# Kernel optimization log

Measured on AMD Instinct MI355X. Metric: run time of the kernel, lower is better.

## Reference

```python
import jax, jax.numpy as jnp
import numpy as np

H = 1024   # hidden_size
NH = 16    # num heads
DH = H // NH
L = 2      # attention levels
E = 8      # experts
F = 4 * H  # expert FFN hidden
B = 2
S = 1024
EPS = 1e-5
TOPK = 2
STD = 0.02


def setup_inputs() -> dict:
    key = jax.random.key(0)
    ks = jax.random.split(key, 12)
    def n(k, shp):
        return jax.random.normal(k, shp, jnp.float32) * STD
    return {
        "hidden_states": jax.random.normal(ks[0], (B, S, H), jnp.float32),
        "attention_mask": jnp.ones((B, S), jnp.int32),
        "ln1_g": jnp.ones((H,), jnp.float32), "ln1_b": jnp.zeros((H,), jnp.float32),
        "ln2_g": jnp.ones((H,), jnp.float32), "ln2_b": jnp.zeros((H,), jnp.float32),
        "Wq": n(ks[1], (L, H, H)), "Wk": n(ks[2], (L, H, H)),
        "Wv": n(ks[3], (L, H, H)), "Wo": n(ks[4], (L, H, H)),
        "bq": jnp.zeros((L, H), jnp.float32), "bk": jnp.zeros((L, H), jnp.float32),
        "bv": jnp.zeros((L, H), jnp.float32), "bo": jnp.zeros((L, H), jnp.float32),
        "level_logits": n(ks[5], (L,)),
        "Wr": n(ks[6], (H, E)), "br": jnp.zeros((E,), jnp.float32),
        "W1": n(ks[7], (E, H, F)), "b1": jnp.zeros((E, F), jnp.float32),
        "W2": n(ks[8], (E, F, H)), "b2": jnp.zeros((E, H), jnp.float32),
    }


def _ln(x, g, b):
    m = x.mean(-1, keepdims=True)
    v = x.var(-1, keepdims=True)
    return (x - m) * jax.lax.rsqrt(v + EPS) * g + b


def _mla(x, mask_f, Wq, Wk, Wv, Wo, bq, bk, bv, bo, level_logits):
    # Multi-level attention: one MHA per level, softmax-combined over levels.
    b_, s_, _ = x.shape
    def proj(W, bias):
        y = jnp.einsum('bsh,lhd->lbsd', x, W) + bias[:, None, None, :]
        return y.reshape(L, b_, s_, NH, DH)
    q, k, v = proj(Wq, bq), proj(Wk, bk), proj(Wv, bv)
    scores = jnp.einsum('lbqnd,lbknd->lbnqk', q, k) / np.float32(np.sqrt(DH))
    bias = (1.0 - mask_f)[None, :, None, None, :] * jnp.float32(-1e9)  # key-side mask
    attn = jax.nn.softmax(scores + bias, axis=-1)
    ctx = jnp.einsum('lbnqk,lbknd->lbqnd', attn, v).reshape(L, b_, s_, H)
    out = jnp.einsum('lbsh,lhd->lbsd', ctx, Wo) + bo[:, None, None, :]
    w = jax.nn.softmax(level_logits)
    return jnp.einsum('l,lbsd->bsd', w, out)


def _moe(x, Wr, br, W1, b1, W2, b2):
    # Top-2 softmax router with renormalized gates; dense expert compute,
    # sparse combine (math-equivalent to dispatch/combine without dropping).
    logits = x @ Wr + br                                  # [B,S,E]
    probs = jax.nn.softmax(logits, axis=-1)
    topv, topi = jax.lax.top_k(probs, TOPK)               # [B,S,K]
    gates = topv / topv.sum(-1, keepdims=True)
    combine = jnp.sum(jax.nn.one_hot(topi, E, dtype=x.dtype) * gates[..., None], axis=-2)  # [B,S,E]
    h = jax.nn.gelu(jnp.einsum('bsh,ehf->besf', x, W1) + b1[None, :, None, :])
    y = jnp.einsum('besf,efh->besh', h, W2) + b2[None, :, None, :]
    return jnp.einsum('bse,besh->bsh', combine, y), logits


def reference(hidden_states, attention_mask, ln1_g, ln1_b, ln2_g, ln2_b,
              Wq, Wk, Wv, Wo, bq, bk, bv, bo, level_logits,
              Wr, br, W1, b1, W2, b2):
    mask_f = attention_mask.astype(jnp.float32)
    attn = _mla(_ln(hidden_states, ln1_g, ln1_b), mask_f,
                Wq, Wk, Wv, Wo, bq, bk, bv, bo, level_logits)
    x = hidden_states + attn                  # residual 1 (dropout in eval = identity)
    moe_out, _router_logits = _moe(_ln(x, ln2_g, ln2_b), Wr, br, W1, b1, W2, b2)
    return x + moe_out                        # residual 2
```

## Files before the change

kernel.cpp:

```cpp
#include <hip/hip_runtime.h>
#include <hip/hip_bf16.h>
#include <stdint.h>

#define Hn   1024
#define NHn  16
#define DHn  64
#define Ln   2
#define En   8
#define Fn   4096
#define Bn   2
#define Sn   1024
#define Tn   2048
#define An   4096
#define KSPLIT 4

typedef __bf16 bf16_t;
typedef __bf16 bf16x2 __attribute__((ext_vector_type(2)));
typedef __bf16 bf16x4 __attribute__((ext_vector_type(4)));
typedef __bf16 bf16x8 __attribute__((ext_vector_type(8)));
typedef float  f32x4  __attribute__((ext_vector_type(4)));

__device__ __forceinline__ f32x4 mfma16(bf16x8 a, bf16x8 b, f32x4 c){
  return __builtin_amdgcn_mfma_f32_16x16x32_bf16(a, b, c, 0, 0, 0);
}
__device__ __forceinline__ void gload16(const void* gsrc, void* ldst){
  __builtin_amdgcn_global_load_lds((const __attribute__((address_space(1))) void*)gsrc,
                                   (__attribute__((address_space(3))) void*)ldst, 16, 0, 0);
}
__device__ __forceinline__ float gelu_f(float x){
  float u = 0.7978845608028654f * (x + 0.044715f * x * x * x);
  return 0.5f * x * (1.0f + tanhf(u));
}

__global__ __launch_bounds__(256)
void tcvt_k(const float* __restrict__ src, bf16_t* __restrict__ dst, int R, int C){
  __shared__ float tile[32][33];
  size_t moff = (size_t)blockIdx.z * R * C;
  src += moff; dst += moff;
  int c0 = blockIdx.x * 32, r0 = blockIdx.y * 32;
  int tx = threadIdx.x & 31, ty = threadIdx.x >> 5;
  #pragma unroll
  for (int i = 0; i < 32; i += 8)
    tile[ty + i][tx] = src[(size_t)(r0 + ty + i) * C + (c0 + tx)];
  __syncthreads();
  #pragma unroll
  for (int i = 0; i < 32; i += 8)
    dst[(size_t)(c0 + ty + i) * R + (r0 + tx)] = (bf16_t)tile[tx][ty + i];
}

__global__ __launch_bounds__(256)
void ln_k(const float* __restrict__ x, const float* __restrict__ gam,
          const float* __restrict__ bet, bf16_t* __restrict__ out){
  int row = blockIdx.x;
  const float4* xr = (const float4*)(x + (size_t)row * Hn);
  int t = threadIdx.x, lane = t & 63, w = t >> 6;
  float4 v = xr[t];
  float s  = v.x + v.y + v.z + v.w;
  float ss = v.x*v.x + v.y*v.y + v.z*v.z + v.w*v.w;
  #pragma unroll
  for (int mk = 1; mk < 64; mk <<= 1){ s += __shfl_xor(s, mk); ss += __shfl_xor(ss, mk); }
  __shared__ float r1[4], r2[4];
  if (lane == 0){ r1[w] = s; r2[w] = ss; }
  __syncthreads();
  float S1 = r1[0]+r1[1]+r1[2]+r1[3];
  float S2 = r2[0]+r2[1]+r2[2]+r2[3];
  float mean = S1 * (1.0f/Hn);
  float var  = S2 * (1.0f/Hn) - mean*mean;
  float rstd = rsqrtf(var + 1e-5f);
  int c = t * 4;
  bf16_t* o = out + (size_t)row * Hn + c;
  o[0] = (bf16_t)((v.x-mean)*rstd*gam[c+0] + bet[c+0]);
  o[1] = (bf16_t)((v.y-mean)*rstd*gam[c+1] + bet[c+1]);
  o[2] = (bf16_t)((v.z-mean)*rstd*gam[c+2] + bet[c+2]);
  o[3] = (bf16_t)((v.w-mean)*rstd*gam[c+3] + bet[c+3]);
}

__global__ __launch_bounds__(256)
void res_ln2_k(const float* __restrict__ x, const float* __restrict__ o0,
               const float* __restrict__ o1, const float* __restrict__ lvl,
               const float* __restrict__ gam, const float* __restrict__ bet,
               float* __restrict__ x2, bf16_t* __restrict__ xn2){
  int row = blockIdx.x, t = threadIdx.x, lane = t & 63, w = t >> 6;
  float l0 = lvl[0], l1 = lvl[1];
  float mx = fmaxf(l0, l1);
  float e0 = __expf(l0 - mx), e1 = __expf(l1 - mx);
  float inv = 1.f / (e0 + e1);
  float w0 = e0 * inv, w1 = e1 * inv;
  size_t base = (size_t)row * Hn;
  float4 xv = ((const float4*)(x  + base))[t];
  float4 a0 = ((const float4*)(o0 + base))[t];
  float4 a1 = ((const float4*)(o1 + base))[t];
  float4 v;
  v.x = xv.x + w0*a0.x + w1*a1.x;
  v.y = xv.y + w0*a0.y + w1*a1.y;
  v.z = xv.z + w0*a0.z + w1*a1.z;
  v.w = xv.w + w0*a0.w + w1*a1.w;
  ((float4*)(x2 + base))[t] = v;
  float s  = v.x + v.y + v.z + v.w;
  float ss = v.x*v.x + v.y*v.y + v.z*v.z + v.w*v.w;
  #pragma unroll
  for (int mk = 1; mk < 64; mk <<= 1){ s += __shfl_xor(s, mk); ss += __shfl_xor(ss, mk); }
  __shared__ float r1[4], r2[4];
  if (lane == 0){ r1[w] = s; r2[w] = ss; }
  __syncthreads();
  float S1 = r1[0]+r1[1]+r1[2]+r1[3];
  float S2 = r2[0]+r2[1]+r2[2]+r2[3];
  float mean = S1 * (1.0f/Hn);
  float var  = S2 * (1.0f/Hn) - mean*mean;
  float rstd = rsqrtf(var + 1e-5f);
  int c = t * 4;
  bf16_t* o = xn2 + base + c;
  o[0] = (bf16_t)((v.x-mean)*rstd*gam[c+0] + bet[c+0]);
  o[1] = (bf16_t)((v.y-mean)*rstd*gam[c+1] + bet[c+1]);
  o[2] = (bf16_t)((v.z-mean)*rstd*gam[c+2] + bet[c+2]);
  o[3] = (bf16_t)((v.w-mean)*rstd*gam[c+3] + bet[c+3]);
}

struct GP {
  const bf16_t* A;
  const bf16_t* Bt;
  const float*  bias;
  float*        fout;
  bf16_t*       bfout;
  const int*    list;
  const int*    counts;
  int Kstride;
  int Kloc;
};

template<int MODE>
__global__ __launch_bounds__(256)
void gemm_k(GP p){
  const int nt = blockIdx.x, mt = blockIdx.y, z = blockIdx.z;
  const bf16_t* A = p.A;
  const bf16_t* Bt = p.Bt;
  const float* bias = p.bias;
  const int* list = nullptr;
  int cnt = 0x7fffffff;
  int kbase = 0;
  if constexpr (MODE == 0){
    Bt += (size_t)z*Hn*Hn; bias += z*Hn;
  } else if constexpr (MODE == 1){
    Bt += (size_t)z*Hn*Hn; bias += z*Hn; A += (size_t)z*Bn*Sn*Hn;
  } else if constexpr (MODE == 3){
    cnt = p.counts[z];
    if (mt * 128 >= cnt) return;
    list = p.list + z * Tn;
    Bt += (size_t)z*Fn*Hn; bias += z*Fn;
  } else {
    int e = z >> 2;
    cnt = p.counts[e];
    if (mt * 128 >= cnt) return;
    list = p.list + e * Tn;
    Bt += (size_t)e*Hn*Fn; bias += e*Hn;
    kbase = (z & 3) * (Fn / KSPLIT);
  }
  const int Ks = p.Kstride;
  const int NT = p.Kloc >> 5;

  __shared__ bf16_t As[2][128*32];
  __shared__ bf16_t Bs[2][128*32];
  const int tid = threadIdx.x, lane = tid & 63, w = tid >> 6;
  const int wr = (w >> 1) * 64, wc = (w & 1) * 64;
  const int lane15 = lane & 15, kg = lane >> 4;

  const bf16_t* aptr[2];
  const bf16_t* bptr[2];
  int chunks[2];
  #pragma unroll
  for (int i = 0; i < 2; ++i){
    int ch = w*64 + lane + i*256;
    chunks[i] = ch;
    int row = ch >> 2, kc = (ch & 3) * 8;
    int ar;
    if constexpr (MODE == 3){ int g = mt*128 + row; if (g >= cnt) g = cnt - 1; ar = list[g] >> 1; }
    else if constexpr (MODE == 4){ int g = mt*128 + row; if (g >= cnt) g = cnt - 1; ar = list[g]; }
    else ar = mt*128 + row;
    aptr[i] = A  + (size_t)ar * Ks + kbase + kc;
    bptr[i] = Bt + (size_t)(nt*128 + row) * Ks + kbase + kc;
  }

  const f32x4 fz = {0.f,0.f,0.f,0.f};
  f32x4 acc[4][4];
  #pragma unroll
  for (int m = 0; m < 4; ++m)
    #pragma unroll
    for (int n = 0; n < 4; ++n) acc[m][n] = fz;

  #pragma unroll
  for (int i = 0; i < 2; ++i){
    gload16(aptr[i], &As[0][chunks[i]*8]);
    gload16(bptr[i], &Bs[0][chunks[i]*8]);
  }
  __syncthreads();

  int cur = 0;
  for (int t = 0; t < NT; ++t){
    if (t + 1 < NT){
      int k1 = (t+1) * 32;
      #pragma unroll
      for (int i = 0; i < 2; ++i){
        gload16(aptr[i] + k1, &As[cur^1][chunks[i]*8]);
        gload16(bptr[i] + k1, &Bs[cur^1][chunks[i]*8]);
      }
    }
    bf16x8 af[4], bfr[4];
    #pragma unroll
    for (int m = 0; m < 4; ++m) af[m]  = *(const bf16x8*)(&As[cur][(wr + m*16 + lane15)*32 + kg*8]);
    #pragma unroll
    for (int n = 0; n < 4; ++n) bfr[n] = *(const bf16x8*)(&Bs[cur][(wc + n*16 + lane15)*32 + kg*8]);
    #pragma unroll
    for (int m = 0; m < 4; ++m)
      #pragma unroll
      for (int n = 0; n < 4; ++n)
        acc[m][n] = mfma16(af[m], bfr[n], acc[m][n]);
    __syncthreads();
    cur ^= 1;
  }

  if constexpr (MODE == 0){
    bf16_t* outp = p.bfout + (size_t)z * (Bn*NHn*Sn*DHn);
    if (z < 4){
      #pragma unroll
      for (int m = 0; m < 4; ++m){
        int row0 = mt*128 + wr + m*16 + kg*4;
        #pragma unroll
        for (int n = 0; n < 4; ++n){
          int col = nt*128 + wc + n*16 + lane15;
          int nh = col >> 6, dh = col & 63;
          float bv = bias[col];
          f32x4 v = acc[m][n];
          #pragma unroll
          for (int r = 0; r < 4; ++r){
            int tk = row0 + r;
            int bb = tk >> 10, s = tk & 1023;
            outp[((size_t)(bb*NHn + nh)*Sn + s)*DHn + dh] = (bf16_t)(v[r] + bv);
          }
        }
      }
    } else {
      #pragma unroll
      for (int m = 0; m < 4; ++m){
        int row0 = mt*128 + wr + m*16 + kg*4;
        int bb = row0 >> 10, s = row0 & 1023;
        #pragma unroll
        for (int n = 0; n < 4; ++n){
          int col = nt*128 + wc + n*16 + lane15;
          int nh = col >> 6, dh = col & 63;
          float bv = bias[col];
          f32x4 v = acc[m][n];
          bf16x4 pk;
          pk[0] = (bf16_t)(v[0] + bv);
          pk[1] = (bf16_t)(v[1] + bv);
          pk[2] = (bf16_t)(v[2] + bv);
          pk[3] = (bf16_t)(v[3] + bv);
          *(bf16x4*)(outp + ((size_t)(bb*NHn + nh)*DHn + dh)*Sn + s) = pk;
        }
      }
    }
  } else if constexpr (MODE == 1){
    float* outp = p.fout + (size_t)z * Tn * Hn;
    #pragma unroll
    for (int m = 0; m < 4; ++m){
      int row0 = mt*128 + wr + m*16 + kg*4;
      #pragma unroll
      for (int n = 0; n < 4; ++n){
        int col = nt*128 + wc + n*16 + lane15;
        float bv = bias[col];
        f32x4 v = acc[m][n];
        #pragma unroll
        for (int r = 0; r < 4; ++r)
          outp[(size_t)(row0 + r)*Hn + col] = v[r] + bv;
      }
    }
  } else if constexpr (MODE == 3){
    #pragma unroll
    for (int m = 0; m < 4; ++m){
      int row0 = mt*128 + wr + m*16 + kg*4;
      #pragma unroll
      for (int n = 0; n < 4; ++n){
        int col = nt*128 + wc + n*16 + lane15;
        float bv = bias[col];
        f32x4 v = acc[m][n];
        #pragma unroll
        for (int r = 0; r < 4; ++r){
          int g = row0 + r;
          if (g < cnt){
            int aid = list[g];
            p.bfout[(size_t)aid*Fn + col] = (bf16_t)gelu_f(v[r] + bv);
          }
        }
      }
    }
  } else {
    float* outp = p.fout + (size_t)(z & 3) * An * Hn;
    bool addb = (z & 3) == 0;
    #pragma unroll
    for (int m = 0; m < 4; ++m){
      int row0 = mt*128 + wr + m*16 + kg*4;
      #pragma unroll
      for (int n = 0; n < 4; ++n){
        int col = nt*128 + wc + n*16 + lane15;
        float bv = addb ? bias[col] : 0.f;
        f32x4 v = acc[m][n];
        #pragma unroll
        for (int r = 0; r < 4; ++r){
          int g = row0 + r;
          if (g < cnt){
            int aid = list[g];
            outp[(size_t)aid*Hn + col] = v[r] + bv;
          }
        }
      }
    }
  }
}

__global__ __launch_bounds__(64)
void attn_k(const bf16_t* __restrict__ qh, const bf16_t* __restrict__ kh,
            const bf16_t* __restrict__ vtb, const int* __restrict__ amask,
            bf16_t* __restrict__ ctxb){
  int z  = blockIdx.x;
  int qt = blockIdx.y;
  int lvl = z >> 5, bb = (z >> 4) & 1, nh = z & 15;
  int lane = threadIdx.x;
  int lane15 = lane & 15, kg = lane >> 4;
  const bf16_t* Q  = qh  + (size_t)z * Sn * DHn;
  const bf16_t* Kp = kh  + (size_t)z * Sn * DHn;
  const bf16_t* Vt = vtb + (size_t)z * DHn * Sn;
  const int* mrow = amask + bb * Sn;
  __shared__ float bias_lds[Sn];
  __shared__ bf16_t p_lds[16*40];
  for (int i = lane; i < Sn/4; i += 64){
    int4 mv = ((const int4*)mrow)[i];
    float4 bv;
    bv.x = mv.x ? 0.f : -1e9f;
    bv.y = mv.y ? 0.f : -1e9f;
    bv.z = mv.z ? 0.f : -1e9f;
    bv.w = mv.w ? 0.f : -1e9f;
    ((float4*)bias_lds)[i] = bv;
  }
  const f32x4 fz = {0.f,0.f,0.f,0.f};
  int qr = qt*16 + lane15;
  bf16x8 qa0 = *(const bf16x8*)(Q + (size_t)qr*DHn + kg*8);
  bf16x8 qa1 = *(const bf16x8*)(Q + (size_t)qr*DHn + 32 + kg*8);
  f32x4 ctxa[4] = {fz, fz, fz, fz};
  float m_ln = -1e30f;
  float s_ln = 0.f;
  float m_out[4] = {-1e30f,-1e30f,-1e30f,-1e30f};
  for (int kc = 0; kc < 32; ++kc){
    int k0 = kc * 32;
    bf16x8 ka0 = *(const bf16x8*)(Kp + (size_t)(k0+lane15)*DHn + kg*8);
    bf16x8 ka1 = *(const bf16x8*)(Kp + (size_t)(k0+lane15)*DHn + 32 + kg*8);
    bf16x8 kb0 = *(const bf16x8*)(Kp + (size_t)(k0+16+lane15)*DHn + kg*8);
    bf16x8 kb1 = *(const bf16x8*)(Kp + (size_t)(k0+16+lane15)*DHn + 32 + kg*8);
    f32x4 sA = mfma16(ka1, qa1, mfma16(ka0, qa0, fz));
    f32x4 sB = mfma16(kb1, qa1, mfma16(kb0, qa0, fz));
    float4 biasA = *(const float4*)(bias_lds + k0 + kg*4);
    float4 biasB = *(const float4*)(bias_lds + k0 + 16 + kg*4);
    float sv[8];
    sv[0] = sA[0]*0.125f + biasA.x;
    sv[1] = sA[1]*0.125f + biasA.y;
    sv[2] = sA[2]*0.125f + biasA.z;
    sv[3] = sA[3]*0.125f + biasA.w;
    sv[4] = sB[0]*0.125f + biasB.x;
    sv[5] = sB[1]*0.125f + biasB.y;
    sv[6] = sB[2]*0.125f + biasB.z;
    sv[7] = sB[3]*0.125f + biasB.w;
    float mx = fmaxf(fmaxf(fmaxf(sv[0],sv[1]),fmaxf(sv[2],sv[3])),
                     fmaxf(fmaxf(sv[4],sv[5]),fmaxf(sv[6],sv[7])));
    mx = fmaxf(mx, __shfl_xor(mx, 16));
    mx = fmaxf(mx, __shfl_xor(mx, 32));
    if (!__all(mx <= m_ln)){
      float mnew = fmaxf(m_ln, mx);
      s_ln *= __expf(m_ln - mnew);
      #pragma unroll
      for (int r = 0; r < 4; ++r){
        float mo = __shfl(mnew, kg*4 + r);
        float corr = __expf(m_out[r] - mo);
        ctxa[0][r] *= corr; ctxa[1][r] *= corr; ctxa[2][r] *= corr; ctxa[3][r] *= corr;
        m_out[r] = mo;
      }
      m_ln = mnew;
    }
    float pv[8];
    #pragma unroll
    for (int j = 0; j < 8; ++j){ pv[j] = __expf(sv[j] - m_ln); s_ln += pv[j]; }
    bf16_t* pr = p_lds + lane15*40;
    *(bf16x2*)(pr + kg*4)          = (bf16x2){(bf16_t)pv[0], (bf16_t)pv[1]};
    *(bf16x2*)(pr + kg*4 + 2)      = (bf16x2){(bf16_t)pv[2], (bf16_t)pv[3]};
    *(bf16x2*)(pr + 16 + kg*4)     = (bf16x2){(bf16_t)pv[4], (bf16_t)pv[5]};
    *(bf16x2*)(pr + 16 + kg*4 + 2) = (bf16x2){(bf16_t)pv[6], (bf16_t)pv[7]};
    bf16x8 paf = *(const bf16x8*)(p_lds + lane15*40 + kg*8);
    #pragma unroll
    for (int df = 0; df < 4; ++df){
      bf16x8 vbf = *(const bf16x8*)(Vt + (size_t)(df*16 + lane15)*Sn + k0 + kg*8);
      ctxa[df] = mfma16(paf, vbf, ctxa[df]);
    }
  }
  s_ln += __shfl_xor(s_ln, 16);
  s_ln += __shfl_xor(s_ln, 32);
  #pragma unroll
  for (int r = 0; r < 4; ++r){
    float inv = 1.f / __shfl(s_ln, kg*4 + r);
    int srow = qt*16 + kg*4 + r;
    #pragma unroll
    for (int df = 0; df < 4; ++df){
      int d = df*16 + lane15;
      ctxb[((size_t)(lvl*2 + bb)*Sn + srow)*Hn + nh*DHn + d] = (bf16_t)(ctxa[df][r] * inv);
    }
  }
}

__global__ __launch_bounds__(64)
void router_k(const float* __restrict__ x2, const float* __restrict__ gam,
              const float* __restrict__ bet, const float* __restrict__ Wr,
              const float* __restrict__ br, float* __restrict__ gates,
              int* __restrict__ lists, int* __restrict__ counts){
  int t = blockIdx.x, lane = threadIdx.x;
  const float4* xr = (const float4*)(x2 + (size_t)t * Hn);
  float4 vbuf[4];
  float s = 0.f, ss = 0.f;
  #pragma unroll
  for (int i = 0; i < 4; ++i){
    float4 v = xr[lane + i*64];
    vbuf[i] = v;
    s  += v.x + v.y + v.z + v.w;
    ss += v.x*v.x + v.y*v.y + v.z*v.z + v.w*v.w;
  }
  #pragma unroll
  for (int mk = 1; mk < 64; mk <<= 1){ s += __shfl_xor(s, mk); ss += __shfl_xor(ss, mk); }
  float mean = s * (1.0f/Hn);
  float var  = ss * (1.0f/Hn) - mean*mean;
  float rstd = rsqrtf(var + 1e-5f);
  float a[8] = {0,0,0,0,0,0,0,0};
  #pragma unroll
  for (int i = 0; i < 4; ++i){
    int c = (lane + i*64) * 4;
    float4 v = vbuf[i];
    float xn[4] = {
      (v.x-mean)*rstd*gam[c+0] + bet[c+0],
      (v.y-mean)*rstd*gam[c+1] + bet[c+1],
      (v.z-mean)*rstd*gam[c+2] + bet[c+2],
      (v.w-mean)*rstd*gam[c+3] + bet[c+3]};
    #pragma unroll
    for (int j = 0; j < 4; ++j){
      const float* w = Wr + (size_t)(c + j) * En;
      #pragma unroll
      for (int e8 = 0; e8 < 8; ++e8) a[e8] += xn[j] * w[e8];
    }
  }
  #pragma unroll
  for (int e8 = 0; e8 < 8; ++e8)
    #pragma unroll
    for (int mk = 1; mk < 64; mk <<= 1) a[e8] += __shfl_xor(a[e8], mk);
  if (lane == 0){
    float lg[8]; float mx = -1e30f;
    #pragma unroll
    for (int e8 = 0; e8 < 8; ++e8){ lg[e8] = a[e8] + br[e8]; mx = fmaxf(mx, lg[e8]); }
    float p[8];
    #pragma unroll
    for (int e8 = 0; e8 < 8; ++e8) p[e8] = __expf(lg[e8] - mx);
    int i0 = 0; float v0 = p[0];
    #pragma unroll
    for (int e8 = 1; e8 < 8; ++e8) if (p[e8] > v0){ v0 = p[e8]; i0 = e8; }
    int i1 = -1; float v1 = -1.f;
    #pragma unroll
    for (int e8 = 0; e8 < 8; ++e8) if (e8 != i0 && p[e8] > v1){ v1 = p[e8]; i1 = e8; }
    float g0 = v0 / (v0 + v1), g1 = v1 / (v0 + v1);
    gates[2*t] = g0; gates[2*t+1] = g1;
    int s0 = atomicAdd(&counts[i0], 1); lists[i0*Tn + s0] = 2*t;
    int s1 = atomicAdd(&counts[i1], 1); lists[i1*Tn + s1] = 2*t + 1;
  }
}

__global__ __launch_bounds__(256)
void comb_k(const float* __restrict__ x2, const float* __restrict__ P,
            const float* __restrict__ gates, float* __restrict__ out){
  int t = blockIdx.x, i = threadIdx.x;
  float g0 = gates[2*t], g1 = gates[2*t+1];
  const size_t PS = (size_t)An * Hn;
  f32x4 s0 = {0,0,0,0}, s1 = {0,0,0,0};
  #pragma unroll
  for (int ks = 0; ks < KSPLIT; ++ks){
    f32x4 u0 = ((const f32x4*)(P + ks*PS + (size_t)(2*t)*Hn))[i];
    f32x4 u1 = ((const f32x4*)(P + ks*PS + (size_t)(2*t+1)*Hn))[i];
    s0 += u0; s1 += u1;
  }
  f32x4 va = ((const f32x4*)(x2 + (size_t)t*Hn))[i];
  f32x4 o = va + g0*s0 + g1*s1;
  ((f32x4*)(out + (size_t)t*Hn))[i] = o;
}

extern "C" void kernel_launch(void* const* d_in, const int* in_sizes, int n_in,
                              void* d_out, int out_size, void* d_ws, size_t ws_size,
                              hipStream_t stream)
{
  const float* x    = (const float*)d_in[0];
  const int* amask  = (const int*)d_in[1];
  const float* ln1g = (const float*)d_in[2];
  const float* ln1b = (const float*)d_in[3];
  const float* ln2g = (const float*)d_in[4];
  const float* ln2b = (const float*)d_in[5];
  const float* Wq   = (const float*)d_in[6];
  const float* Wk   = (const float*)d_in[7];
  const float* Wv   = (const float*)d_in[8];
  const float* Wo   = (const float*)d_in[9];
  const float* bq   = (const float*)d_in[10];
  const float* bk   = (const float*)d_in[11];
  const float* bv   = (const float*)d_in[12];
  const float* bo   = (const float*)d_in[13];
  const float* lvl  = (const float*)d_in[14];
  const float* Wr   = (const float*)d_in[15];
  const float* br   = (const float*)d_in[16];
  const float* W1   = (const float*)d_in[17];
  const float* b1   = (const float*)d_in[18];
  const float* W2   = (const float*)d_in[19];
  const float* b2   = (const float*)d_in[20];
  float* out = (float*)d_out;
  (void)in_sizes; (void)n_in; (void)out_size; (void)ws_size;

  char* wsp = (char*)d_ws;
  auto nxt = [&](size_t bytes) -> char* {
    char* r = wsp; wsp += (bytes + 255) & ~(size_t)255; return r;
  };
  bf16_t* wqkvT = (bf16_t*)nxt((size_t)6*Hn*Hn*2);
  bf16_t* woT   = (bf16_t*)nxt((size_t)Ln*Hn*Hn*2);
  bf16_t* w1t   = (bf16_t*)nxt((size_t)En*Fn*Hn*2);
  bf16_t* w2t   = (bf16_t*)nxt((size_t)En*Hn*Fn*2);
  float*  bqkv  = (float*)nxt((size_t)6*Hn*4);
  bf16_t* xn1   = (bf16_t*)nxt((size_t)Tn*Hn*2);
  bf16_t* qkvh  = (bf16_t*)nxt((size_t)6*Bn*NHn*Sn*DHn*2);
  bf16_t* ctxb  = (bf16_t*)nxt((size_t)Ln*Bn*Sn*Hn*2);
  float*  otmp  = (float*)nxt((size_t)Ln*Tn*Hn*4);
  float*  x2    = (float*)nxt((size_t)Tn*Hn*4);
  bf16_t* xn2   = (bf16_t*)nxt((size_t)Tn*Hn*2);
  float*  gates = (float*)nxt((size_t)Tn*2*4);
  int*    lists = (int*)nxt((size_t)En*Tn*4);
  int*    counts= (int*)nxt(256);
  bf16_t* hbuf  = (bf16_t*)nxt((size_t)An*Fn*2);
  float*  ybuf  = (float*)nxt((size_t)KSPLIT*An*Hn*4);

  hipMemsetAsync(counts, 0, En*sizeof(int), stream);
  hipMemcpyAsync(bqkv,          bq, (size_t)Ln*Hn*4, hipMemcpyDeviceToDevice, stream);
  hipMemcpyAsync(bqkv + 2*Hn,   bk, (size_t)Ln*Hn*4, hipMemcpyDeviceToDevice, stream);
  hipMemcpyAsync(bqkv + 4*Hn,   bv, (size_t)Ln*Hn*4, hipMemcpyDeviceToDevice, stream);

  tcvt_k<<<dim3(32,32,Ln), 256, 0, stream>>>(Wq, wqkvT,            Hn, Hn);
  tcvt_k<<<dim3(32,32,Ln), 256, 0, stream>>>(Wk, wqkvT + 2*Hn*Hn,  Hn, Hn);
  tcvt_k<<<dim3(32,32,Ln), 256, 0, stream>>>(Wv, wqkvT + 4*Hn*Hn,  Hn, Hn);
  tcvt_k<<<dim3(32,32,Ln), 256, 0, stream>>>(Wo, woT,              Hn, Hn);
  tcvt_k<<<dim3(Fn/32, Hn/32, En), 256, 0, stream>>>(W1, w1t, Hn, Fn);
  tcvt_k<<<dim3(Hn/32, Fn/32, En), 256, 0, stream>>>(W2, w2t, Fn, Hn);

  ln_k<<<Tn, 256, 0, stream>>>(x, ln1g, ln1b, xn1);

  { GP g{};
    g.A = xn1; g.Bt = wqkvT; g.bias = bqkv; g.bfout = qkvh;
    g.Kstride = Hn; g.Kloc = Hn;
    gemm_k<0><<<dim3(8,16,6), 256, 0, stream>>>(g); }

  {
    const bf16_t* qh = qkvh;
    const bf16_t* kh = qkvh + (size_t)2*Bn*NHn*Sn*DHn;
    const bf16_t* vt = qkvh + (size_t)4*Bn*NHn*Sn*DHn;
    attn_k<<<dim3(Ln*Bn*NHn, Sn/16), 64, 0, stream>>>(qh, kh, vt, amask, ctxb);
  }

  { GP g{};
    g.A = ctxb; g.Bt = woT; g.bias = bo; g.fout = otmp;
    g.Kstride = Hn; g.Kloc = Hn;
    gemm_k<1><<<dim3(8,16,2), 256, 0, stream>>>(g); }

  res_ln2_k<<<Tn, 256, 0, stream>>>(x, otmp, otmp + (size_t)Tn*Hn, lvl,
                                    ln2g, ln2b, x2, xn2);
  router_k<<<Tn, 64, 0, stream>>>(x2, ln2g, ln2b, Wr, br, gates, lists, counts);

  { GP g{};
    g.A = xn2; g.Bt = w1t; g.bias = b1; g.bfout = hbuf;
    g.list = lists; g.counts = counts;
    g.Kstride = Hn; g.Kloc = Hn;
    gemm_k<3><<<dim3(Fn/128, 16, En), 256, 0, stream>>>(g); }
  { GP g{};
    g.A = hbuf; g.Bt = w2t; g.bias = b2; g.fout = ybuf;
    g.list = lists; g.counts = counts;
    g.Kstride = Fn; g.Kloc = Fn / KSPLIT;
    gemm_k<4><<<dim3(Hn/128, 16, En*KSPLIT), 256, 0, stream>>>(g); }

  comb_k<<<Tn, 256, 0, stream>>>(x2, ybuf, gates, out);
}
```

Baseline: 560.1 us.

## Share K/V tiles across four waves via double-buffered swizzled LDS in attention

The attention kernel goes from one wave per 16-query tile to four waves per block covering 64 queries. Each 32-key chunk of K and V is loaded once into XOR-swizzled shared memory and reused by all four waves, with double buffering so the next chunk's load overlaps compute. This cuts redundant global/L2 reads of K and V by about four times. The cost is a block-wide barrier every iteration and more LDS per block, which may lower occupancy.

After: 489.2 us. 1.15x faster.

```diff
diff --git a/kernel.cpp b/kernel.cpp
--- a/kernel.cpp
+++ b/kernel.cpp
@@ -316,31 +316,41 @@
   }
 }
 
-__global__ __launch_bounds__(64)
+__global__ __launch_bounds__(256)
 void attn_k(const bf16_t* __restrict__ qh, const bf16_t* __restrict__ kh,
             const bf16_t* __restrict__ vtb, const int* __restrict__ amask,
             bf16_t* __restrict__ ctxb){
   int z  = blockIdx.x;
-  int qt = blockIdx.y;
+  int qb = blockIdx.y;
   int lvl = z >> 5, bb = (z >> 4) & 1, nh = z & 15;
-  int lane = threadIdx.x;
+  int tid = threadIdx.x, lane = tid & 63, w = tid >> 6;
   int lane15 = lane & 15, kg = lane >> 4;
   const bf16_t* Q  = qh  + (size_t)z * Sn * DHn;
   const bf16_t* Kp = kh  + (size_t)z * Sn * DHn;
   const bf16_t* Vt = vtb + (size_t)z * DHn * Sn;
   const int* mrow = amask + bb * Sn;
+  __shared__ bf16_t Ks[2][32*64];
+  __shared__ bf16_t Vs[2][64*32];
   __shared__ float bias_lds[Sn];
-  __shared__ bf16_t p_lds[16*40];
-  for (int i = lane; i < Sn/4; i += 64){
-    int4 mv = ((const int4*)mrow)[i];
+  __shared__ bf16_t p_lds[4][16*40];
+  {
+    int4 mv = ((const int4*)mrow)[tid];
     float4 bv;
     bv.x = mv.x ? 0.f : -1e9f;
     bv.y = mv.y ? 0.f : -1e9f;
     bv.z = mv.z ? 0.f : -1e9f;
     bv.w = mv.w ? 0.f : -1e9f;
-    ((float4*)bias_lds)[i] = bv;
-  }
+    ((float4*)bias_lds)[tid] = bv;
+  }
+  int krow = w*8 + (lane >> 3);
+  const bf16_t* ksrc = Kp + (size_t)krow*DHn + (((lane&7) ^ (krow&7)) << 3);
+  int vrow = w*16 + (lane >> 2);
+  const bf16_t* vsrc = Vt + (size_t)vrow*Sn + ((((lane&3) ^ ((vrow>>2)&3))) << 3);
+  bf16_t* kdst[2] = { &Ks[0][w*512 + lane*8], &Ks[1][w*512 + lane*8] };
+  bf16_t* vdst[2] = { &Vs[0][w*512 + lane*8], &Vs[1][w*512 + lane*8] };
+
   const f32x4 fz = {0.f,0.f,0.f,0.f};
+  int qt = qb*4 + w;
   int qr = qt*16 + lane15;
   bf16x8 qa0 = *(const bf16x8*)(Q + (size_t)qr*DHn + kg*8);
   bf16x8 qa1 = *(const bf16x8*)(Q + (size_t)qr*DHn + 32 + kg*8);
@@ -348,12 +358,31 @@
   float m_ln = -1e30f;
   float s_ln = 0.f;
   float m_out[4] = {-1e30f,-1e30f,-1e30f,-1e30f};
+
+  const int kslot0 = (kg ^ (lane15 & 7));
+  const int kslot1 = ((kg + 4) ^ (lane15 & 7));
+  const int ka_off0 = lane15*64 + kslot0*8;
+  const int ka_off1 = lane15*64 + kslot1*8;
+  const int kb_off0 = (16 + lane15)*64 + kslot0*8;
+  const int kb_off1 = (16 + lane15)*64 + kslot1*8;
+
+  gload16(ksrc, kdst[0]);
+  gload16(vsrc, vdst[0]);
+  __syncthreads();
+
   for (int kc = 0; kc < 32; ++kc){
+    const int cur = kc & 1;
+    const bf16_t* Kb = Ks[cur];
+    const bf16_t* Vb = Vs[cur];
+    if (kc + 1 < 32){
+      gload16(ksrc + (size_t)(kc+1)*32*DHn, kdst[cur^1]);
+      gload16(vsrc + (kc+1)*32,             vdst[cur^1]);
+    }
     int k0 = kc * 32;
-    bf16x8 ka0 = *(const bf16x8*)(Kp + (size_t)(k0+lane15)*DHn + kg*8);
-    bf16x8 ka1 = *(const bf16x8*)(Kp + (size_t)(k0+lane15)*DHn + 32 + kg*8);
-    bf16x8 kb0 = *(const bf16x8*)(Kp + (size_t)(k0+16+lane15)*DHn + kg*8);
-    bf16x8 kb1 = *(const bf16x8*)(Kp + (size_t)(k0+16+lane15)*DHn + 32 + kg*8);
+    bf16x8 ka0 = *(const bf16x8*)(Kb + ka_off0);
+    bf16x8 ka1 = *(const bf16x8*)(Kb + ka_off1);
+    bf16x8 kb0 = *(const bf16x8*)(Kb + kb_off0);
+    bf16x8 kb1 = *(const bf16x8*)(Kb + kb_off1);
     f32x4 sA = mfma16(ka1, qa1, mfma16(ka0, qa0, fz));
     f32x4 sB = mfma16(kb1, qa1, mfma16(kb0, qa0, fz));
     float4 biasA = *(const float4*)(bias_lds + k0 + kg*4);
@@ -386,17 +415,19 @@
     float pv[8];
     #pragma unroll
     for (int j = 0; j < 8; ++j){ pv[j] = __expf(sv[j] - m_ln); s_ln += pv[j]; }
-    bf16_t* pr = p_lds + lane15*40;
+    bf16_t* pr = p_lds[w] + lane15*40;
     *(bf16x2*)(pr + kg*4)          = (bf16x2){(bf16_t)pv[0], (bf16_t)pv[1]};
     *(bf16x2*)(pr + kg*4 + 2)      = (bf16x2){(bf16_t)pv[2], (bf16_t)pv[3]};
     *(bf16x2*)(pr + 16 + kg*4)     = (bf16x2){(bf16_t)pv[4], (bf16_t)pv[5]};
     *(bf16x2*)(pr + 16 + kg*4 + 2) = (bf16x2){(bf16_t)pv[6], (bf16_t)pv[7]};
-    bf16x8 paf = *(const bf16x8*)(p_lds + lane15*40 + kg*8);
+    bf16x8 paf = *(const bf16x8*)(p_lds[w] + lane15*40 + kg*8);
     #pragma unroll
     for (int df = 0; df < 4; ++df){
-      bf16x8 vbf = *(const bf16x8*)(Vt + (size_t)(df*16 + lane15)*Sn + k0 + kg*8);
+      int r = df*16 + lane15;
+      bf16x8 vbf = *(const bf16x8*)(Vb + r*32 + ((kg ^ ((r>>2)&3)) << 3));
       ctxa[df] = mfma16(paf, vbf, ctxa[df]);
     }
+    __syncthreads();
   }
   s_ln += __shfl_xor(s_ln, 16);
   s_ln += __shfl_xor(s_ln, 32);
@@ -564,7 +595,7 @@
     const bf16_t* qh = qkvh;
     const bf16_t* kh = qkvh + (size_t)2*Bn*NHn*Sn*DHn;
     const bf16_t* vt = qkvh + (size_t)4*Bn*NHn*Sn*DHn;
-    attn_k<<<dim3(Ln*Bn*NHn, Sn/16), 64, 0, stream>>>(qh, kh, vt, amask, ctxb);
+    attn_k<<<dim3(Ln*Bn*NHn, Sn/64), 256, 0, stream>>>(qh, kh, vt, amask, ctxb);
   }
 
   { GP g{};
```
